# Kernel optimization log

Hardware: AMD Instinct MI355X
Metric: run time of the kernel (lower is better)

The kernel has to match this reference:

```python
import jax, jax.numpy as jnp
import numpy as np

N_NODES = 200000
N_EVENTS = 150000
MEM_DIM = 128
RAW_DIM = 128
TIME_DIM = 128
MSG_DIM = 2 * MEM_DIM + RAW_DIM + TIME_DIM  # 512, IdentityMessage out_channels


def setup_inputs() -> dict:
    key = jax.random.key(0)
    ks = jax.random.split(key, 10)
    memory = jax.random.normal(ks[0], (N_NODES, MEM_DIM), jnp.float32)
    last_update = jax.random.randint(ks[1], (N_NODES,), 0, 1000, jnp.int32)
    src = jax.random.randint(ks[2], (N_EVENTS,), 0, N_NODES, jnp.int32)
    dst = jax.random.randint(ks[3], (N_EVENTS,), 0, N_NODES, jnp.int32)
    t = jax.random.randint(ks[4], (N_EVENTS,), 0, 100000, jnp.int32)
    raw_msg = jax.random.normal(ks[5], (N_EVENTS, RAW_DIM), jnp.float32)
    time_w = jax.random.normal(ks[6], (TIME_DIM,), jnp.float32) * 0.05
    time_b = jax.random.normal(ks[7], (TIME_DIM,), jnp.float32) * 0.05
    W_ih = jax.random.normal(ks[8], (3 * MEM_DIM, MSG_DIM), jnp.float32) * (1.0 / np.sqrt(MSG_DIM))
    W_hh = jax.random.normal(ks[9], (3 * MEM_DIM, MEM_DIM), jnp.float32) * (1.0 / np.sqrt(MEM_DIM))
    b_ih = jnp.zeros((3 * MEM_DIM,), jnp.float32)
    b_hh = jnp.zeros((3 * MEM_DIM,), jnp.float32)
    return {"memory": memory, "last_update": last_update, "src": src, "dst": dst,
            "t": t, "raw_msg": raw_msg, "time_w": time_w, "time_b": time_b,
            "W_ih": W_ih, "W_hh": W_hh, "b_ih": b_ih, "b_hh": b_hh}


def reference(memory, last_update, src, dst, t, raw_msg, time_w, time_b, W_ih, W_hh, b_ih, b_hh):
    N = memory.shape[0]

    def compute_msg(s, d):
        # t_rel = t - last_update[src]; time enc = cos(Linear(1->time_dim)(t_rel))
        t_rel = (t - last_update[s]).astype(memory.dtype)
        t_enc = jnp.cos(t_rel[:, None] * time_w[None, :] + time_b[None, :])
        # IdentityMessage: concat(mem[src], mem[dst], raw_msg, t_enc)  -> [E, MSG_DIM]
        return jnp.concatenate([memory[s], memory[d], raw_msg, t_enc], axis=-1)

    msg_s = compute_msg(src, dst)   # source-direction store
    msg_d = compute_msg(dst, src)   # destination-direction store (edges reversed)
    idx = jnp.concatenate([src, dst])          # destination node of each message
    msg = jnp.concatenate([msg_s, msg_d], axis=0)
    tt = jnp.concatenate([t, t])

    # MeanAggregator: segment-mean of messages per destination node
    sums = jax.ops.segment_sum(msg, idx, num_segments=N)
    cnt = jax.ops.segment_sum(jnp.ones_like(tt, dtype=msg.dtype), idx, num_segments=N)
    aggr = sums / jnp.maximum(cnt, 1.0)[:, None]

    # GRUCell(aggr, memory)
    gi = aggr @ W_ih.T + b_ih
    gh = memory @ W_hh.T + b_hh
    i_r, i_z, i_n = jnp.split(gi, 3, axis=-1)
    h_r, h_z, h_n = jnp.split(gh, 3, axis=-1)
    r = jax.nn.sigmoid(i_r + h_r)
    z = jax.nn.sigmoid(i_z + h_z)
    n = jnp.tanh(i_n + r * h_n)
    new_memory = (1.0 - z) * n + z * memory

    # last_update = scatter(t, idx, reduce='max') over all nodes
    new_last_update = jnp.zeros((N,), tt.dtype).at[idx].max(tt)
    return new_memory, new_last_update
```

## Files before the change

### kernel.cpp

```cpp
#include <hip/hip_runtime.h>
#include <cstdint>


#define MEMD 128
#define ACCD 384
#define MSGD 512

typedef __attribute__((ext_vector_type(8))) short bf16x8;
typedef __attribute__((ext_vector_type(2))) short bf16x2;
typedef __attribute__((ext_vector_type(4))) float f32x4;

static __device__ __forceinline__ short f2bf(float f) {
    uint32_t u = __builtin_bit_cast(uint32_t, f);
    u = (u + 0x7FFFu + ((u >> 16) & 1u)) >> 16;
    return (short)u;
}
static __device__ __forceinline__ float bf2f(short s) {
    return __builtin_bit_cast(float, ((uint32_t)(uint16_t)s) << 16);
}
static __device__ __forceinline__ void load_lds16(const void* g, void* l) {
    __builtin_amdgcn_global_load_lds(
        (const __attribute__((address_space(1))) unsigned int*)g,
        (__attribute__((address_space(3))) unsigned int*)l,
        16, 0, 0);
}

__global__ __launch_bounds__(256) void tgn_prep_mem(
    const float* __restrict__ mem, short* __restrict__ memB, int n8)
{
    const int i = blockIdx.x * 256 + threadIdx.x;
    if (i >= n8) return;
    const float4 a = *reinterpret_cast<const float4*>(mem + (size_t)i * 8);
    const float4 b = *reinterpret_cast<const float4*>(mem + (size_t)i * 8 + 4);
    bf16x8 v;
    v[0] = f2bf(a.x); v[1] = f2bf(a.y); v[2] = f2bf(a.z); v[3] = f2bf(a.w);
    v[4] = f2bf(b.x); v[5] = f2bf(b.y); v[6] = f2bf(b.z); v[7] = f2bf(b.w);
    *reinterpret_cast<bf16x8*>(memB + (size_t)i * 8) = v;
}

#define GI_SLOTS (24 * 16 * 64)
#define GH_SLOTS (24 * 4 * 64)

__global__ __launch_bounds__(256) void tgn_prep_w(
    const float* __restrict__ W_ih, const float* __restrict__ W_hh,
    bf16x8* __restrict__ Wb)
{
    const int s = blockIdx.x * 256 + threadIdx.x;
    if (s >= GI_SLOTS + GH_SLOTS) return;
    const float* src;
    if (s < GI_SLOTS) {
        const int n = s / (16 * 64), rem = s % (16 * 64);
        const int ks = rem / 64, l = rem % 64;
        const int j = n * 16 + (l & 15), k = ks * 32 + (l >> 4) * 8;
        src = W_ih + (size_t)j * MSGD + k;
    } else {
        const int s2 = s - GI_SLOTS;
        const int n = s2 / (4 * 64), rem = s2 % (4 * 64);
        const int ks = rem / 64, l = rem % 64;
        const int j = n * 16 + (l & 15), k = ks * 32 + (l >> 4) * 8;
        src = W_hh + (size_t)j * MEMD + k;
    }
    bf16x8 v;
    #pragma unroll
    for (int e = 0; e < 8; ++e) v[e] = f2bf(src[e]);
    Wb[s] = v;
}

__global__ __launch_bounds__(256) void tgn_fill(
    const int* __restrict__ src, const int* __restrict__ dst, const int* __restrict__ t,
    int* __restrict__ head, int* __restrict__ nxt, int* __restrict__ lu_new,
    int n_events)
{
    const int e = blockIdx.x * 256 + threadIdx.x;
    if (e >= n_events) return;
    const int s = src[e];
    const int d = dst[e];
    const int te = t[e];
    nxt[2 * e]     = atomicExch(head + s, 2 * e);
    nxt[2 * e + 1] = atomicExch(head + d, 2 * e + 1);
    atomicMax(lu_new + s, te);
    atomicMax(lu_new + d, te);
}

__global__ __launch_bounds__(256) void tgn_aggregate(
    const int* __restrict__ head, const int* __restrict__ nxt,
    const int* __restrict__ src, const int* __restrict__ dst, const int* __restrict__ t,
    const float* __restrict__ raw_msg, const short* __restrict__ memB,
    const int* __restrict__ last_update,
    const float* __restrict__ time_w, const float* __restrict__ time_b,
    short* __restrict__ ACC, const int* __restrict__ lu, float* __restrict__ out2,
    int n_nodes)
{
    const int n = blockIdx.x * 4 + (threadIdx.x >> 6);
    if (n >= n_nodes) return;
    const int lane = threadIdx.x & 63;
    if (lane == 0) out2[n] = (float)lu[n];
    int k = head[n];
    if (k < 0) return;
    const int j0 = lane * 2;

    const float lus = (float)last_update[n];
    const float2 tw = *reinterpret_cast<const float2*>(time_w + j0);
    const float2 tb = *reinterpret_cast<const float2*>(time_b + j0);

    float am0 = 0.f, am1 = 0.f, ar0 = 0.f, ar1 = 0.f, at0 = 0.f, at1 = 0.f;
    int c = 0;
    while (k >= 0) {
        const int kn = nxt[k];
        const int e = k >> 1;
        const int other = (k & 1) ? src[e] : dst[e];
        const float te = (float)t[e];
        const float2 rw = *reinterpret_cast<const float2*>(raw_msg + (size_t)e * MEMD + j0);
        const bf16x2 mb = *reinterpret_cast<const bf16x2*>(memB + (size_t)other * MEMD + j0);
        const float dt = te - lus;
        at0 += __cosf(fmaf(dt, tw.x, tb.x));
        at1 += __cosf(fmaf(dt, tw.y, tb.y));
        ar0 += rw.x; ar1 += rw.y;
        am0 += bf2f(mb[0]); am1 += bf2f(mb[1]);
        ++c;
        k = kn;
    }
    const float inv = 1.0f / (float)c;
    short* row = ACC + (size_t)n * ACCD;
    bf16x2 v;
    v[0] = f2bf(am0 * inv); v[1] = f2bf(am1 * inv);
    *reinterpret_cast<bf16x2*>(row + j0) = v;
    v[0] = f2bf(ar0 * inv); v[1] = f2bf(ar1 * inv);
    *reinterpret_cast<bf16x2*>(row + 128 + j0) = v;
    v[0] = f2bf(at0 * inv); v[1] = f2bf(at1 * inv);
    *reinterpret_cast<bf16x2*>(row + 256 + j0) = v;
}

#define WPTR(NN, S) ((S) < 4 ? (Wh + (size_t)((NN) * 4 + (S)) * 64 + lane)      \
                             : (Wb + (size_t)((NN) * 16 + (S) - 4) * 64 + lane))

#define MFMA2(ACCN, BV)                                                          \
    ACCN[0] = __builtin_amdgcn_mfma_f32_16x16x32_bf16(a0, BV, ACCN[0], 0, 0, 0); \
    ACCN[1] = __builtin_amdgcn_mfma_f32_16x16x32_bf16(a1, BV, ACCN[1], 0, 0, 0);

#define STEP(S, B0, B1, B2, ACCARR)                                              \
    {                                                                            \
        const int ks_ = (S) < 4 ? (S) : (S) - 4;                                 \
        const bf16x8 a0 = Xf[(0 * 16 + ks_) * 64 + lane];                        \
        const bf16x8 a1 = Xf[(1 * 16 + ks_) * 64 + lane];                        \
        MFMA2(ACCARR[0], B0)                                                     \
        MFMA2(ACCARR[1], B1)                                                     \
        MFMA2(ACCARR[2], B2)                                                     \
    }                                                                            \
    if ((S) + 3 < 20) {                                                          \
        B0 = *WPTR(n0, (S) + 3);                                                 \
        B1 = *WPTR(n1, (S) + 3);                                                 \
        B2 = *WPTR(n2, (S) + 3);                                                 \
    }

__global__ __launch_bounds__(512, 4) void tgn_gru_mfma(
    const short* __restrict__ memB, const short* __restrict__ ACC,
    const int* __restrict__ head, const bf16x8* __restrict__ Wb,
    const float* __restrict__ b_ih, const float* __restrict__ b_hh,
    float* __restrict__ out, int n_nodes)
{
    __shared__ bf16x8 Xf[2 * 16 * 64];
    ushort* Xh = reinterpret_cast<ushort*>(Xf);
    float*  Sout = reinterpret_cast<float*>(Xf);

    const int tid = threadIdx.x;
    const int lane = tid & 63;
    const int wv = tid >> 6;
    const int node0 = blockIdx.x * 32;

    const bf16x8* __restrict__ Wh = Wb + GI_SLOTS;
    const int n0 = wv, n1 = wv + 8, n2 = wv + 16;

    #pragma unroll
    for (int i = 0; i < 4; ++i) {
        const int slotbase = i * 512 + (tid & ~63);
        const int slot = slotbase + lane;
        const int ks = (slot >> 6) & 15;
        const int m = slot >> 10;
        int node = node0 + m * 16 + (lane & 15);
        if (node >= n_nodes) node = n_nodes - 1;
        const int kbase = ks * 32 + (lane >> 4) * 8;
        const short* g = (kbase < 128)
            ? (memB + (size_t)node * MEMD + kbase)
            : (ACC + (size_t)node * ACCD + (kbase - 128));
        load_lds16(g, &Xf[slotbase]);
    }

    bf16x8 rA0 = *WPTR(n0, 0), rA1 = *WPTR(n1, 0), rA2 = *WPTR(n2, 0);
    bf16x8 rB0 = *WPTR(n0, 1), rB1 = *WPTR(n1, 1), rB2 = *WPTR(n2, 1);
    bf16x8 rC0 = *WPTR(n0, 2), rC1 = *WPTR(n1, 2), rC2 = *WPTR(n2, 2);

    asm volatile("s_waitcnt vmcnt(0)" ::: "memory");
    __syncthreads();

    const int col = lane & 15;
    const int rgrp = lane >> 4;

    uint32_t hmask = 0;
    #pragma unroll
    for (int m = 0; m < 2; ++m)
        #pragma unroll
        for (int r = 0; r < 4; ++r) {
            const int node = node0 + m * 16 + rgrp * 4 + r;
            if (node < n_nodes && head[node] >= 0) hmask |= 1u << (m * 4 + r);
        }

    f32x4 acc_i[3][2], acc_h[3][2];
    #pragma unroll
    for (int c = 0; c < 3; ++c)
        #pragma unroll
        for (int m = 0; m < 2; ++m) {
            acc_i[c][m] = (f32x4){0.f, 0.f, 0.f, 0.f};
            acc_h[c][m] = (f32x4){0.f, 0.f, 0.f, 0.f};
        }

    STEP(0,  rA0, rA1, rA2, acc_h)
    STEP(1,  rB0, rB1, rB2, acc_h)
    STEP(2,  rC0, rC1, rC2, acc_h)
    STEP(3,  rA0, rA1, rA2, acc_h)
    STEP(4,  rB0, rB1, rB2, acc_i)
    STEP(5,  rC0, rC1, rC2, acc_i)
    STEP(6,  rA0, rA1, rA2, acc_i)
    STEP(7,  rB0, rB1, rB2, acc_i)
    STEP(8,  rC0, rC1, rC2, acc_i)
    STEP(9,  rA0, rA1, rA2, acc_i)
    STEP(10, rB0, rB1, rB2, acc_i)
    STEP(11, rC0, rC1, rC2, acc_i)
    STEP(12, rA0, rA1, rA2, acc_i)
    STEP(13, rB0, rB1, rB2, acc_i)
    STEP(14, rC0, rC1, rC2, acc_i)
    STEP(15, rA0, rA1, rA2, acc_i)
    STEP(16, rB0, rB1, rB2, acc_i)
    STEP(17, rC0, rC1, rC2, acc_i)
    STEP(18, rA0, rA1, rA2, acc_i)
    STEP(19, rB0, rB1, rB2, acc_i)

    const int jr = wv * 16 + col;
    const float bir = b_ih[jr], biz = b_ih[jr + 128], bin = b_ih[jr + 256];
    const float bhr = b_hh[jr], bhz = b_hh[jr + 128], bhn = b_hh[jr + 256];
    const int ksj = jr >> 5;
    const int sub = ((jr >> 3) & 3) * 16;
    const int elem = jr & 7;

    float rout[2][4];
    #pragma unroll
    for (int m = 0; m < 2; ++m) {
        #pragma unroll
        for (int r = 0; r < 4; ++r) {
            const bool has = (hmask >> (m * 4 + r)) & 1;
            const float gir = (has ? acc_i[0][m][r] : 0.f) + bir;
            const float giz = (has ? acc_i[1][m][r] : 0.f) + biz;
            const float gin = (has ? acc_i[2][m][r] : 0.f) + bin;
            const float ghr = acc_h[0][m][r] + bhr;
            const float ghz = acc_h[1][m][r] + bhz;
            const float ghn = acc_h[2][m][r] + bhn;
            const float rr = __fdividef(1.0f, 1.0f + __expf(-(gir + ghr)));
            const float zz = __fdividef(1.0f, 1.0f + __expf(-(giz + ghz)));
            const float targ = fmaf(rr, ghn, gin);
            const float e2v = __expf(2.0f * targ);
            const float nn = __fdividef(e2v - 1.0f, e2v + 1.0f);
            const int slot = (m * 16 + ksj) * 64 + sub + (rgrp * 4 + r);
            const float mv = bf2f((short)Xh[slot * 8 + elem]);
            rout[m][r] = (1.0f - zz) * nn + zz * mv;
        }
    }
    __syncthreads();

    #pragma unroll
    for (int m = 0; m < 2; ++m)
        #pragma unroll
        for (int r = 0; r < 4; ++r)
            Sout[(m * 16 + rgrp * 4 + r) * MEMD + jr] = rout[m][r];
    __syncthreads();

    float4* out4 = reinterpret_cast<float4*>(out + (size_t)node0 * MEMD);
    const float4* S4 = reinterpret_cast<const float4*>(Sout);
    if (node0 + 32 <= n_nodes) {
        #pragma unroll
        for (int it = 0; it < 2; ++it)
            out4[it * 512 + tid] = S4[it * 512 + tid];
    } else {
        #pragma unroll
        for (int it = 0; it < 2; ++it) {
            const int idx = it * 512 + tid;
            if (node0 + (idx >> 5) < n_nodes) out4[idx] = S4[idx];
        }
    }
}

extern "C" void kernel_launch(void* const* d_in, const int* in_sizes, int n_in,
                              void* d_out, int out_size, void* d_ws, size_t ws_size,
                              hipStream_t stream)
{
    const float* memory      = (const float*)d_in[0];
    const int*   last_update = (const int*)d_in[1];
    const int*   src         = (const int*)d_in[2];
    const int*   dst         = (const int*)d_in[3];
    const int*   t           = (const int*)d_in[4];
    const float* raw_msg     = (const float*)d_in[5];
    const float* time_w      = (const float*)d_in[6];
    const float* time_b      = (const float*)d_in[7];
    const float* W_ih        = (const float*)d_in[8];
    const float* W_hh        = (const float*)d_in[9];
    const float* b_ih        = (const float*)d_in[10];
    const float* b_hh        = (const float*)d_in[11];

    const int n_nodes  = in_sizes[0] / MEMD;
    const int n_events = in_sizes[2];

    short* ACC  = (short*)d_ws;
    int*   head = (int*)(ACC + (size_t)n_nodes * ACCD);
    int*   nxt  = head + n_nodes;
    int*   lu   = nxt + 2 * n_events;
    bf16x8* Wb  = (bf16x8*)(lu + n_nodes);
    short* memB = (short*)(Wb + GI_SLOTS + GH_SLOTS);

    (void)hipMemsetAsync(head, 0xFF, (size_t)n_nodes * sizeof(int), stream);
    (void)hipMemsetAsync(lu, 0, (size_t)n_nodes * sizeof(int), stream);

    tgn_prep_w<<<dim3((GI_SLOTS + GH_SLOTS + 255) / 256), dim3(256), 0, stream>>>(W_ih, W_hh, Wb);

    const int n8 = n_nodes * MEMD / 8;
    tgn_prep_mem<<<dim3((n8 + 255) / 256), dim3(256), 0, stream>>>(memory, memB, n8);

    tgn_fill<<<dim3((n_events + 255) / 256), dim3(256), 0, stream>>>(
        src, dst, t, head, nxt, lu, n_events);

    float* out2 = (float*)d_out + (size_t)n_nodes * MEMD;
    tgn_aggregate<<<dim3((n_nodes + 3) / 4), dim3(256), 0, stream>>>(
        head, nxt, src, dst, t, raw_msg, memB, last_update, time_w, time_b,
        ACC, lu, out2, n_nodes);

    tgn_gru_mfma<<<dim3((n_nodes + 31) / 32), dim3(512), 0, stream>>>(
        memB, ACC, head, Wb, b_ih, b_hh, (float*)d_out, n_nodes);
}
```

Before: 375.5 us.

## Fuse per-node message aggregation into GRU MFMA kernel via LDS staging

Removes the separate aggregation kernel and its bf16 ACC workspace. Each wave of the GRU block now walks the linked event lists for 4 of the block's 32 nodes and writes the mean memory, raw-message and time-encoding features as packed bf16 straight into the LDS operand tile used by the MFMAs. This avoids the global write and re-read of the 384-wide aggregate rows and one kernel launch. In exchange, the irregular pointer-chasing gather now sits inside the MFMA kernel, which runs 512-thread blocks under a tighter launch-bounds occupancy limit, so latency hiding for the gather may suffer.

```diff
diff --git a/kernel.cpp b/kernel.cpp
--- a/kernel.cpp
+++ b/kernel.cpp
@@ -17,6 +17,9 @@
 }
 static __device__ __forceinline__ float bf2f(short s) {
     return __builtin_bit_cast(float, ((uint32_t)(uint16_t)s) << 16);
+}
+static __device__ __forceinline__ uint32_t pack2bf(float a, float b) {
+    return (uint32_t)(uint16_t)f2bf(a) | ((uint32_t)(uint16_t)f2bf(b) << 16);
 }
 static __device__ __forceinline__ void load_lds16(const void* g, void* l) {
     __builtin_amdgcn_global_load_lds(
@@ -82,55 +85,6 @@
     atomicMax(lu_new + d, te);
 }
 
-__global__ __launch_bounds__(256) void tgn_aggregate(
-    const int* __restrict__ head, const int* __restrict__ nxt,
-    const int* __restrict__ src, const int* __restrict__ dst, const int* __restrict__ t,
-    const float* __restrict__ raw_msg, const short* __restrict__ memB,
-    const int* __restrict__ last_update,
-    const float* __restrict__ time_w, const float* __restrict__ time_b,
-    short* __restrict__ ACC, const int* __restrict__ lu, float* __restrict__ out2,
-    int n_nodes)
-{
-    const int n = blockIdx.x * 4 + (threadIdx.x >> 6);
-    if (n >= n_nodes) return;
-    const int lane = threadIdx.x & 63;
-    if (lane == 0) out2[n] = (float)lu[n];
-    int k = head[n];
-    if (k < 0) return;
-    const int j0 = lane * 2;
-
-    const float lus = (float)last_update[n];
-    const float2 tw = *reinterpret_cast<const float2*>(time_w + j0);
-    const float2 tb = *reinterpret_cast<const float2*>(time_b + j0);
-
-    float am0 = 0.f, am1 = 0.f, ar0 = 0.f, ar1 = 0.f, at0 = 0.f, at1 = 0.f;
-    int c = 0;
-    while (k >= 0) {
-        const int kn = nxt[k];
-        const int e = k >> 1;
-        const int other = (k & 1) ? src[e] : dst[e];
-        const float te = (float)t[e];
-        const float2 rw = *reinterpret_cast<const float2*>(raw_msg + (size_t)e * MEMD + j0);
-        const bf16x2 mb = *reinterpret_cast<const bf16x2*>(memB + (size_t)other * MEMD + j0);
-        const float dt = te - lus;
-        at0 += __cosf(fmaf(dt, tw.x, tb.x));
-        at1 += __cosf(fmaf(dt, tw.y, tb.y));
-        ar0 += rw.x; ar1 += rw.y;
-        am0 += bf2f(mb[0]); am1 += bf2f(mb[1]);
-        ++c;
-        k = kn;
-    }
-    const float inv = 1.0f / (float)c;
-    short* row = ACC + (size_t)n * ACCD;
-    bf16x2 v;
-    v[0] = f2bf(am0 * inv); v[1] = f2bf(am1 * inv);
-    *reinterpret_cast<bf16x2*>(row + j0) = v;
-    v[0] = f2bf(ar0 * inv); v[1] = f2bf(ar1 * inv);
-    *reinterpret_cast<bf16x2*>(row + 128 + j0) = v;
-    v[0] = f2bf(at0 * inv); v[1] = f2bf(at1 * inv);
-    *reinterpret_cast<bf16x2*>(row + 256 + j0) = v;
-}
-
 #define WPTR(NN, S) ((S) < 4 ? (Wh + (size_t)((NN) * 4 + (S)) * 64 + lane)      \
                              : (Wb + (size_t)((NN) * 16 + (S) - 4) * 64 + lane))
 
@@ -153,14 +107,21 @@
         B2 = *WPTR(n2, (S) + 3);                                                 \
     }
 
-__global__ __launch_bounds__(512, 4) void tgn_gru_mfma(
-    const short* __restrict__ memB, const short* __restrict__ ACC,
-    const int* __restrict__ head, const bf16x8* __restrict__ Wb,
+__global__ __launch_bounds__(512, 4) void tgn_gru_fused(
+    const short* __restrict__ memB, const int* __restrict__ head,
+    const int* __restrict__ nxt,
+    const int* __restrict__ src, const int* __restrict__ dst,
+    const int* __restrict__ t, const float* __restrict__ raw_msg,
+    const int* __restrict__ last_update,
+    const float* __restrict__ time_w, const float* __restrict__ time_b,
+    const bf16x8* __restrict__ Wb,
     const float* __restrict__ b_ih, const float* __restrict__ b_hh,
-    float* __restrict__ out, int n_nodes)
+    const int* __restrict__ lu, float* __restrict__ out,
+    float* __restrict__ out2, int n_nodes)
 {
     __shared__ bf16x8 Xf[2 * 16 * 64];
     ushort* Xh = reinterpret_cast<ushort*>(Xf);
+    uint32_t* X32 = reinterpret_cast<uint32_t*>(Xf);
     float*  Sout = reinterpret_cast<float*>(Xf);
 
     const int tid = threadIdx.x;
@@ -171,24 +132,62 @@
     const bf16x8* __restrict__ Wh = Wb + GI_SLOTS;
     const int n0 = wv, n1 = wv + 8, n2 = wv + 16;
 
-    #pragma unroll
-    for (int i = 0; i < 4; ++i) {
-        const int slotbase = i * 512 + (tid & ~63);
-        const int slot = slotbase + lane;
-        const int ks = (slot >> 6) & 15;
-        const int m = slot >> 10;
+    {
+        const int m = wv >> 2, ks = wv & 3;
+        const int slotbase = (m * 16 + ks) * 64;
         int node = node0 + m * 16 + (lane & 15);
         if (node >= n_nodes) node = n_nodes - 1;
         const int kbase = ks * 32 + (lane >> 4) * 8;
-        const short* g = (kbase < 128)
-            ? (memB + (size_t)node * MEMD + kbase)
-            : (ACC + (size_t)node * ACCD + (kbase - 128));
-        load_lds16(g, &Xf[slotbase]);
+        load_lds16(memB + (size_t)node * MEMD + kbase, &Xf[slotbase]);
     }
 
     bf16x8 rA0 = *WPTR(n0, 0), rA1 = *WPTR(n1, 0), rA2 = *WPTR(n2, 0);
     bf16x8 rB0 = *WPTR(n0, 1), rB1 = *WPTR(n1, 1), rB2 = *WPTR(n2, 1);
     bf16x8 rC0 = *WPTR(n0, 2), rC1 = *WPTR(n1, 2), rC2 = *WPTR(n2, 2);
+
+    {
+        const int j0 = lane * 2;
+        const float2 tw = *reinterpret_cast<const float2*>(time_w + j0);
+        const float2 tb = *reinterpret_cast<const float2*>(time_b + j0);
+        #pragma unroll
+        for (int q = 0; q < 4; ++q) {
+            const int n = node0 + wv * 4 + q;
+            if (n >= n_nodes) break;
+            int k = head[n];
+            if (k < 0) continue;
+            const float lus = (float)last_update[n];
+            float am0 = 0.f, am1 = 0.f, ar0 = 0.f, ar1 = 0.f, at0 = 0.f, at1 = 0.f;
+            int c = 0;
+            while (k >= 0) {
+                const int kn = nxt[k];
+                const int e = k >> 1;
+                const int other = (k & 1) ? src[e] : dst[e];
+                const float te = (float)t[e];
+                const float2 rw = *reinterpret_cast<const float2*>(raw_msg + (size_t)e * MEMD + j0);
+                const bf16x2 mb = *reinterpret_cast<const bf16x2*>(memB + (size_t)other * MEMD + j0);
+                const float dt = te - lus;
+                at0 += __cosf(fmaf(dt, tw.x, tb.x));
+                at1 += __cosf(fmaf(dt, tw.y, tb.y));
+                ar0 += rw.x; ar1 += rw.y;
+                am0 += bf2f(mb[0]); am1 += bf2f(mb[1]);
+                ++c;
+                k = kn;
+            }
+            const float inv = 1.0f / (float)c;
+            const int nn_ = wv * 4 + q;
+            const int mn = nn_ >> 4, nif = nn_ & 15;
+            #pragma unroll
+            for (int p = 0; p < 3; ++p) {
+                const int cc = 128 + p * 128 + j0;
+                const int ks = cc >> 5;
+                const int hi = (cc >> 3) & 3;
+                const int u32idx = ((mn * 16 + ks) * 64 + hi * 16 + nif) * 4 + (lane & 3);
+                const float v0 = (p == 0 ? am0 : p == 1 ? ar0 : at0) * inv;
+                const float v1 = (p == 0 ? am1 : p == 1 ? ar1 : at1) * inv;
+                X32[u32idx] = pack2bf(v0, v1);
+            }
+        }
+    }
 
     asm volatile("s_waitcnt vmcnt(0)" ::: "memory");
     __syncthreads();
@@ -264,6 +263,7 @@
             rout[m][r] = (1.0f - zz) * nn + zz * mv;
         }
     }
+    if (tid < 32 && node0 + tid < n_nodes) out2[node0 + tid] = (float)lu[node0 + tid];
     __syncthreads();
 
     #pragma unroll
@@ -308,8 +308,7 @@
     const int n_nodes  = in_sizes[0] / MEMD;
     const int n_events = in_sizes[2];
 
-    short* ACC  = (short*)d_ws;
-    int*   head = (int*)(ACC + (size_t)n_nodes * ACCD);
+    int*   head = (int*)d_ws;
     int*   nxt  = head + n_nodes;
     int*   lu   = nxt + 2 * n_events;
     bf16x8* Wb  = (bf16x8*)(lu + n_nodes);
@@ -327,10 +326,7 @@
         src, dst, t, head, nxt, lu, n_events);
 
     float* out2 = (float*)d_out + (size_t)n_nodes * MEMD;
-    tgn_aggregate<<<dim3((n_nodes + 3) / 4), dim3(256), 0, stream>>>(
-        head, nxt, src, dst, t, raw_msg, memB, last_update, time_w, time_b,
-        ACC, lu, out2, n_nodes);
-
-    tgn_gru_mfma<<<dim3((n_nodes + 31) / 32), dim3(512), 0, stream>>>(
-        memB, ACC, head, Wb, b_ih, b_hh, (float*)d_out, n_nodes);
-}
+    tgn_gru_fused<<<dim3((n_nodes + 31) / 32), dim3(512), 0, stream>>>(
+        memB, head, nxt, src, dst, t, raw_msg, last_update, time_w, time_b,
+        Wb, b_ih, b_hh, lu, (float*)d_out, out2, n_nodes);
+}
```

New measurement: 334.3 us. 11.0% less time.
